# Kernel tuning notes

Hardware: AMD Instinct MI355X
Metric: run time of the kernel (lower is better)

The kernel has to match this reference:

```python
import math
import jax, jax.numpy as jnp
import numpy as np

MAX_T = 300
B, T, V, D, H = 16, 256, 25, 128, 8


def _layernorm(x, g, b):
    m = x.mean(-1, keepdims=True)
    var = ((x - m) ** 2).mean(-1, keepdims=True)
    return (x - m) / jnp.sqrt(var + 1e-5) * g + b


def setup_inputs() -> dict:
    key = jax.random.key(0)
    ks = jax.random.split(key, 8)
    d = D // H
    init = lambda k, shape: jax.random.normal(k, shape, dtype=jnp.float32) * 0.02
    return dict(
        x=jax.random.normal(ks[0], (B, T, V, D), dtype=jnp.float32),
        ln1_g=jnp.ones((D,), jnp.float32), ln1_b=jnp.zeros((D,), jnp.float32),
        qkv_w=init(ks[1], (D, 3 * D)), qkv_b=jnp.zeros((3 * D,), jnp.float32),
        proj_w=init(ks[2], (D, D)), proj_b=jnp.zeros((D,), jnp.float32),
        logit_scale=jnp.full((H, 1, 1), math.log(math.sqrt(d)), dtype=jnp.float32),
        rel_pos_bias=init(ks[3], (H, 2 * MAX_T - 1)),
        ln2_g=jnp.ones((D,), jnp.float32), ln2_b=jnp.zeros((D,), jnp.float32),
        ffn_w1=init(ks[4], (D, 4 * D)), ffn_b1=jnp.zeros((4 * D,), jnp.float32),
        ffn_w2=init(ks[5], (4 * D, D)), ffn_b2=jnp.zeros((D,), jnp.float32),
    )


def reference(x, ln1_g, ln1_b, qkv_w, qkv_b, proj_w, proj_b, logit_scale,
              rel_pos_bias, ln2_g, ln2_b, ffn_w1, ffn_b1, ffn_w2, ffn_b2):
    b, t, v_, dm = x.shape
    h = logit_scale.shape[0]
    d = dm // h
    # (B, T, V, D) -> (B*V, T, D): attention runs over frames per joint
    xf = x.transpose(0, 2, 1, 3).reshape(b * v_, t, dm)
    res = xf
    xn = _layernorm(xf, ln1_g, ln1_b)
    qkv = (xn @ qkv_w + qkv_b).reshape(b * v_, t, 3, h, d).transpose(2, 0, 3, 1, 4)
    q, k, v = qkv[0], qkv[1], qkv[2]  # (BV, h, T, d)
    scale = jnp.exp(jnp.minimum(logit_scale, math.log(100.0)))  # (h,1,1)
    qn = q / jnp.maximum(jnp.linalg.norm(q, axis=-1, keepdims=True), 1e-12) * scale
    kn = k / jnp.maximum(jnp.linalg.norm(k, axis=-1, keepdims=True), 1e-12)
    # learned relative-position bias, gathered to (h, T, T)
    coords = jnp.arange(t)
    rel = coords[:, None] - coords[None, :] + (MAX_T - 1)
    bias = rel_pos_bias[:, rel]
    # SDPA applies its default 1/sqrt(head_dim) scale on top of logit_scale
    scores = jnp.einsum('bhtd,bhsd->bhts', qn, kn) / math.sqrt(d) + bias[None]
    attn = jax.nn.softmax(scores, axis=-1)
    out = jnp.einsum('bhts,bhsd->bhtd', attn, v)
    out = out.transpose(0, 2, 1, 3).reshape(b * v_, t, dm)
    xf = res + (out @ proj_w + proj_b)
    y = _layernorm(xf, ln2_g, ln2_b)
    y = jax.nn.gelu(y @ ffn_w1 + ffn_b1, approximate=False) @ ffn_w2 + ffn_b2
    xf = xf + y
    return xf.reshape(b, v_, t, dm).transpose(0, 2, 1, 3)
```

## Files before the change

### kernel.cpp

```cpp
#include <hip/hip_runtime.h>
#include <hip/hip_fp16.h>
#include <math.h>

#define B_   16
#define T_   256
#define V_   25
#define D_   128
#define H_   8
#define DH   16
#define BV_  (B_*V_)
#define MAXT 300
#define NREL (2*MAXT-1)
#define LOG2E 1.44269504088896f

typedef __attribute__((ext_vector_type(8))) short short8;
typedef __attribute__((ext_vector_type(4))) float f32x4;
typedef __attribute__((ext_vector_type(2))) __fp16 fp16x2;
typedef __attribute__((ext_vector_type(4))) _Float16 half4;
typedef __attribute__((ext_vector_type(8))) _Float16 half8;

__device__ inline short f2bf(float f) {
  union { float f; unsigned u; } a; a.f = f;
  unsigned r = (a.u + 0x7FFF + ((a.u >> 16) & 1)) >> 16;
  return (short)r;
}

__device__ inline float fast_exp2(float x) {
#if __has_builtin(__builtin_amdgcn_exp2f)
  return __builtin_amdgcn_exp2f(x);
#else
  return exp2f(x);
#endif
}

__device__ inline float gelu_fast(float u) {
  float s = u * fmaf(0.0713548162726f, u*u, 1.5957691216057f);
  return u * __builtin_amdgcn_rcpf(1.0f + __expf(-s));
}

__global__ __launch_bounds__(256) void k0_prep(
    const float* __restrict__ qkv_w, const float* __restrict__ pw,
    const float* __restrict__ w1,    const float* __restrict__ w2,
    short* __restrict__ qkv_wt, short* __restrict__ pwt,
    _Float16* __restrict__ w1t, _Float16* __restrict__ w2t)
{
  int i = blockIdx.x*256 + threadIdx.x;
  if (i < 384*128) { int n = i >> 7, k = i & 127; qkv_wt[i] = f2bf(qkv_w[k*384 + n]); }
  if (i < 128*128) { int n = i >> 7, k = i & 127; pwt[i]    = f2bf(pw[k*128 + n]); }
  if (i < 512*128) { int n = i >> 7, k = i & 127; w1t[i]    = (_Float16)w1[k*512 + n]; }
  if (i < 128*512) {
    int r = i & 3, lane = (i >> 2) & 63, hn = (i >> 8) & 31, ot = i >> 13;
    int k = hn*16 + (lane >> 4)*4 + r;
    int n = ot*16 + (lane & 15);
    w2t[i] = (_Float16)w2[k*128 + n];
  }
}

__global__ __launch_bounds__(256) void k1_ln_qkv(
    const float* __restrict__ x, const float* __restrict__ g1, const float* __restrict__ b1,
    const short* __restrict__ qkv_wt, const float* __restrict__ qkv_b,
    const float* __restrict__ logit_scale,
    _Float16* __restrict__ qb, _Float16* __restrict__ kb, _Float16* __restrict__ vt)
{
  __shared__ short xn[64][136];
  const int tid = threadIdx.x;
  const int bv  = blockIdx.x / (T_/64);
  const int t0  = (blockIdx.x % (T_/64)) * 64;
  const int b   = bv / V_, v = bv % V_;

  {
    const int j = tid & 15;
    float4 gA = *(const float4*)(g1 + j*8), gB = *(const float4*)(g1 + j*8 + 4);
    float4 bA = *(const float4*)(b1 + j*8), bB = *(const float4*)(b1 + j*8 + 4);
    float gg[8] = {gA.x,gA.y,gA.z,gA.w,gB.x,gB.y,gB.z,gB.w};
    float bb[8] = {bA.x,bA.y,bA.z,bA.w,bB.x,bB.y,bB.z,bB.w};
    for (int rep = 0; rep < 4; ++rep) {
      const int tok = rep*16 + (tid >> 4);
      const float* xp = x + (((size_t)b*T_ + (t0+tok))*V_ + v)*D_ + j*8;
      float4 a0 = *(const float4*)xp;
      float4 a1 = *(const float4*)(xp+4);
      float e[8] = {a0.x,a0.y,a0.z,a0.w,a1.x,a1.y,a1.z,a1.w};
      float s = 0.f;
      #pragma unroll
      for (int q = 0; q < 8; ++q) s += e[q];
      #pragma unroll
      for (int m = 1; m < 16; m <<= 1) s += __shfl_xor(s, m, 16);
      float mean = s * (1.0f/128.0f);
      float s2 = 0.f;
      #pragma unroll
      for (int q = 0; q < 8; ++q) { float d = e[q]-mean; s2 += d*d; }
      #pragma unroll
      for (int m = 1; m < 16; m <<= 1) s2 += __shfl_xor(s2, m, 16);
      float rstd = rsqrtf(s2*(1.0f/128.0f) + 1e-5f);
      short8 o;
      #pragma unroll
      for (int q = 0; q < 8; ++q) o[q] = f2bf((e[q]-mean)*rstd*gg[q] + bb[q]);
      *(short8*)&xn[tok][j*8] = o;
    }
  }
  __syncthreads();

  const int wave = tid >> 6, lane = tid & 63;
  const int col = lane & 15, quad = lane >> 4;
  short8 af[4][4];
  #pragma unroll
  for (int tt = 0; tt < 4; ++tt)
    #pragma unroll
    for (int kk = 0; kk < 4; ++kk)
      af[tt][kk] = *(const short8*)&xn[tt*16+col][kk*32 + quad*8];

  for (int it = 0; it < 6; ++it) {
    const int tile = wave*6 + it;
    const int n0 = tile*16;
    short8 bf[4];
    #pragma unroll
    for (int kk = 0; kk < 4; ++kk)
      bf[kk] = *(const short8*)(qkv_wt + (size_t)(n0+col)*128 + kk*32 + quad*8);
    f32x4 acc[4] = {{0.f,0.f,0.f,0.f},{0.f,0.f,0.f,0.f},{0.f,0.f,0.f,0.f},{0.f,0.f,0.f,0.f}};
    #pragma unroll
    for (int kk = 0; kk < 4; ++kk)
      #pragma unroll
      for (int tt = 0; tt < 4; ++tt)
        acc[tt] = __builtin_amdgcn_mfma_f32_16x16x32_bf16(af[tt][kk], bf[kk], acc[tt], 0, 0, 0);
    const float bias = qkv_b[n0+col];
    const int h = tile & 7;
    const size_t bh = (size_t)bv*H_ + h;
    if (tile < 16) {
      const float scale = (tile < 8)
        ? __expf(fminf(logit_scale[h], 4.605170185988091f)) * 0.25f * LOG2E : 1.0f;
      #pragma unroll
      for (int tt = 0; tt < 4; ++tt) {
        float val[4], inv[4];
        #pragma unroll
        for (int r = 0; r < 4; ++r) {
          val[r] = acc[tt][r] + bias;
          float s = val[r]*val[r];
          #pragma unroll
          for (int m = 1; m < 16; m <<= 1) s += __shfl_xor(s, m, 16);
          inv[r] = 1.0f / fmaxf(sqrtf(s), 1e-12f);
        }
        const size_t obase = (bh*T_ + (t0 + tt*16 + quad*4))*DH + col;
        if (tile < 8) {
          #pragma unroll
          for (int r = 0; r < 4; ++r) qb[obase + (size_t)r*DH] = (_Float16)(val[r]*inv[r]*scale);
        } else {
          #pragma unroll
          for (int r = 0; r < 4; ++r) kb[obase + (size_t)r*DH] = (_Float16)(val[r]*inv[r]);
        }
      }
    } else {
      #pragma unroll
      for (int tt = 0; tt < 4; ++tt) {
        half4 vh;
        #pragma unroll
        for (int r = 0; r < 4; ++r) vh[r] = (_Float16)(acc[tt][r] + bias);
        *(half4*)(vt + bh*4096 + (size_t)(t0/16 + tt)*256 + col*16 + quad*4) = vh;
      }
    }
  }
}

__global__ __launch_bounds__(256) void k2_attn(
    const float* __restrict__ rel_pos_bias,
    const _Float16* __restrict__ qb, const _Float16* __restrict__ kb,
    const _Float16* __restrict__ vt, short* __restrict__ xattn)
{
  __shared__ float bias_s[NREL + 1];
  const int tid = threadIdx.x;
  const int bh  = blockIdx.x;
  const int h   = bh & (H_-1);
  const int bv  = bh >> 3;
  for (int j = tid; j < NREL; j += 256) bias_s[j] = rel_pos_bias[h*NREL + j] * LOG2E;
  __syncthreads();

  const int wave = tid >> 6, lane = tid & 63;
  const int nn = lane & 15, quad = lane >> 4;
  const size_t qkbase = (size_t)bh * (T_*DH);
  const size_t vbase  = (size_t)bh * 4096;

  half4 qf[4];
  #pragma unroll
  for (int tt = 0; tt < 4; ++tt)
    qf[tt] = *(const half4*)(qb + qkbase + (size_t)(wave*64 + tt*16 + nn)*DH + quad*4);

  f32x4 o[4];
  #pragma unroll
  for (int tt = 0; tt < 4; ++tt) o[tt] = (f32x4){0.f,0.f,0.f,0.f};
  float lsum[4] = {0.f,0.f,0.f,0.f};

  half4 kf = *(const half4*)(kb + qkbase + (size_t)nn*DH + quad*4);
  half4 vf = *(const half4*)(vt + vbase + (size_t)nn*16 + quad*4);

  for (int s16 = 0; s16 < 16; ++s16) {
    half4 kf_n, vf_n;
    if (s16 < 15) {
      kf_n = *(const half4*)(kb + qkbase + (size_t)((s16+1)*16 + nn)*DH + quad*4);
      vf_n = *(const half4*)(vt + vbase + (size_t)(s16+1)*256 + nn*16 + quad*4);
    }
    #pragma unroll
    for (int tt = 0; tt < 4; ++tt) {
      f32x4 c = {0.f,0.f,0.f,0.f};
      c = __builtin_amdgcn_mfma_f32_16x16x16f16(kf, qf[tt], c, 0, 0, 0);
      const int ib = (wave*64 + tt*16 + nn) - (s16*16 + quad*4) + (MAXT-1);
      float p0 = fast_exp2(c[0] + bias_s[ib]);
      float p1 = fast_exp2(c[1] + bias_s[ib - 1]);
      float p2 = fast_exp2(c[2] + bias_s[ib - 2]);
      float p3 = fast_exp2(c[3] + bias_s[ib - 3]);
      lsum[tt] += (p0 + p1) + (p2 + p3);
      fp16x2 lo = __builtin_amdgcn_cvt_pkrtz(p0, p1);
      fp16x2 hi = __builtin_amdgcn_cvt_pkrtz(p2, p3);
      union { struct { fp16x2 a, b; } p; half4 h; } cv;
      cv.p.a = lo; cv.p.b = hi;
      o[tt] = __builtin_amdgcn_mfma_f32_16x16x16f16(cv.h, vf, o[tt], 0, 0, 0);
    }
    kf = kf_n; vf = vf_n;
  }

  #pragma unroll
  for (int tt = 0; tt < 4; ++tt) {
    float l = lsum[tt];
    l += __shfl_xor(l, 16);
    l += __shfl_xor(l, 32);
    float rinv = 1.0f / l;
    #pragma unroll
    for (int r = 0; r < 4; ++r) {
      float inv = __shfl(rinv, quad*4 + r, 16);
      const int t = wave*64 + tt*16 + quad*4 + r;
      xattn[((size_t)bv*T_ + t)*D_ + h*DH + nn] = f2bf(o[tt][r] * inv);
    }
  }
}

__global__ __launch_bounds__(256) void k3_proj(
    const float* __restrict__ x, const short* __restrict__ xattn,
    const short* __restrict__ pwt, const float* __restrict__ proj_b,
    float* __restrict__ xf2)
{
  const int tid = threadIdx.x;
  const int bv  = blockIdx.x / (T_/64);
  const int t0  = (blockIdx.x % (T_/64)) * 64;
  const int b   = bv / V_, v = bv % V_;
  const int wave = tid >> 6, lane = tid & 63;
  const int col = lane & 15, quad = lane >> 4;

  short8 af[4][4];
  #pragma unroll
  for (int tt = 0; tt < 4; ++tt)
    #pragma unroll
    for (int kk = 0; kk < 4; ++kk)
      af[tt][kk] = *(const short8*)(xattn
                    + ((size_t)bv*T_ + t0 + tt*16 + col)*D_ + kk*32 + quad*8);

  for (int it = 0; it < 2; ++it) {
    const int n0 = (wave*2 + it)*16;
    short8 bf[4];
    #pragma unroll
    for (int kk = 0; kk < 4; ++kk)
      bf[kk] = *(const short8*)(pwt + (size_t)(n0+col)*128 + kk*32 + quad*8);
    f32x4 acc[4] = {{0.f,0.f,0.f,0.f},{0.f,0.f,0.f,0.f},{0.f,0.f,0.f,0.f},{0.f,0.f,0.f,0.f}};
    #pragma unroll
    for (int kk = 0; kk < 4; ++kk)
      #pragma unroll
      for (int tt = 0; tt < 4; ++tt)
        acc[tt] = __builtin_amdgcn_mfma_f32_16x16x32_bf16(af[tt][kk], bf[kk], acc[tt], 0, 0, 0);
    const float pbv = proj_b[n0+col];
    #pragma unroll
    for (int tt = 0; tt < 4; ++tt)
      #pragma unroll
      for (int r = 0; r < 4; ++r) {
        const int t = t0 + tt*16 + quad*4 + r;
        float res = x[(((size_t)b*T_ + t)*V_ + v)*D_ + n0 + col];
        xf2[((size_t)bv*T_ + t)*D_ + n0 + col] = acc[tt][r] + pbv + res;
      }
  }
}

__global__ __launch_bounds__(256) void k4_ffn(
    const float* __restrict__ xf2, const float* __restrict__ g2, const float* __restrict__ b2,
    const _Float16* __restrict__ w1t, const float* __restrict__ fb1,
    const _Float16* __restrict__ w2t, const float* __restrict__ fb2,
    float* __restrict__ out)
{
  __shared__ __align__(16) char smem[34816];
  _Float16 (*y_s)[136] = (_Float16 (*)[136])smem;
  _Float16 (*w1c)[136] = (_Float16 (*)[136])smem;
  _Float16 *w2c = (_Float16*)(smem + 64*136*2);

  const int tid = threadIdx.x;
  const int bv  = blockIdx.x / (T_/128);
  const int t0  = (blockIdx.x % (T_/128)) * 128;
  const int b   = bv / V_, v = bv % V_;

  half8 p_w1[4], p_w2[4];
  #pragma unroll
  for (int j = 0; j < 4; ++j) {
    const int u = j*256 + tid;
    p_w1[j] = *(const half8*)(w1t + (size_t)(u >> 4)*128 + (u & 15)*8);
    p_w2[j] = *(const half8*)(w2t + (size_t)((u >> 7)*32 + ((u >> 5) & 3))*256 + (u & 31)*8);
  }

  {
    const int j = tid & 15;
    float4 gA = *(const float4*)(g2 + j*8), gB = *(const float4*)(g2 + j*8 + 4);
    float4 bA = *(const float4*)(b2 + j*8), bB = *(const float4*)(b2 + j*8 + 4);
    float gg[8] = {gA.x,gA.y,gA.z,gA.w,gB.x,gB.y,gB.z,gB.w};
    float bb[8] = {bA.x,bA.y,bA.z,bA.w,bB.x,bB.y,bB.z,bB.w};
    for (int rep = 0; rep < 8; ++rep) {
      const int tok = rep*16 + (tid >> 4);
      const float* xp = xf2 + ((size_t)bv*T_ + t0+tok)*D_ + j*8;
      float4 a0 = *(const float4*)xp;
      float4 a1 = *(const float4*)(xp+4);
      float e[8] = {a0.x,a0.y,a0.z,a0.w,a1.x,a1.y,a1.z,a1.w};
      float s = 0.f;
      #pragma unroll
      for (int q = 0; q < 8; ++q) s += e[q];
      #pragma unroll
      for (int m = 1; m < 16; m <<= 1) s += __shfl_xor(s, m, 16);
      float mean = s * (1.0f/128.0f);
      float s2 = 0.f;
      #pragma unroll
      for (int q = 0; q < 8; ++q) { float d = e[q]-mean; s2 += d*d; }
      #pragma unroll
      for (int m = 1; m < 16; m <<= 1) s2 += __shfl_xor(s2, m, 16);
      float rstd = rsqrtf(s2*(1.0f/128.0f) + 1e-5f);
      half8 o;
      #pragma unroll
      for (int q = 0; q < 8; ++q) o[q] = (_Float16)((e[q]-mean)*rstd*gg[q] + bb[q]);
      *(half8*)&y_s[tok][j*8] = o;
    }
  }
  __syncthreads();

  const int wave = tid >> 6, lane = tid & 63;
  const int col = lane & 15, quad = lane >> 4;

  half8 yf[2][4];
  #pragma unroll
  for (int tt = 0; tt < 2; ++tt)
    #pragma unroll
    for (int kk = 0; kk < 4; ++kk)
      yf[tt][kk] = *(const half8*)&y_s[wave*32 + tt*16 + col][kk*32 + quad*8];
  __syncthreads();

  f32x4 acc2[2][8];
  #pragma unroll
  for (int tt = 0; tt < 2; ++tt)
    #pragma unroll
    for (int ot = 0; ot < 8; ++ot) acc2[tt][ot] = (f32x4){0.f,0.f,0.f,0.f};

  for (int c = 0; c < 8; ++c) {
    #pragma unroll
    for (int j = 0; j < 4; ++j) {
      const int u = j*256 + tid;
      *(half8*)&w1c[u >> 4][(u & 15)*8] = p_w1[j];
      *(half8*)&w2c[(size_t)u*8]        = p_w2[j];
    }
    __syncthreads();

    if (c < 7) {
      #pragma unroll
      for (int j = 0; j < 4; ++j) {
        const int u = j*256 + tid;
        p_w1[j] = *(const half8*)(w1t + (size_t)((c+1)*64 + (u >> 4))*128 + (u & 15)*8);
        p_w2[j] = *(const half8*)(w2t + (size_t)((u >> 7)*32 + (c+1)*4 + ((u >> 5) & 3))*256 + (u & 31)*8);
      }
    }

    #pragma unroll
    for (int ht = 0; ht < 4; ++ht) {
      half8 w1f[4];
      #pragma unroll
      for (int kk = 0; kk < 4; ++kk)
        w1f[kk] = *(const half8*)&w1c[ht*16+col][kk*32 + quad*8];
      f32x4 c0 = {0.f,0.f,0.f,0.f}, c1 = {0.f,0.f,0.f,0.f};
      #pragma unroll
      for (int kk = 0; kk < 4; ++kk) {
        c0 = __builtin_amdgcn_mfma_f32_16x16x32_f16(w1f[kk], yf[0][kk], c0, 0, 0, 0);
        c1 = __builtin_amdgcn_mfma_f32_16x16x32_f16(w1f[kk], yf[1][kk], c1, 0, 0, 0);
      }
      const int hn = c*4 + ht;
      const f32x4 b1v = *(const f32x4*)(fb1 + hn*16 + quad*4);
      half4 pa0, pa1;
      #pragma unroll
      for (int r = 0; r < 4; ++r) {
        pa0[r] = (_Float16)gelu_fast(c0[r] + b1v[r]);
        pa1[r] = (_Float16)gelu_fast(c1[r] + b1v[r]);
      }
      #pragma unroll
      for (int ot = 0; ot < 8; ++ot) {
        half4 w2f = *(const half4*)&w2c[((ot*4 + ht)*64 + lane)*4];
        acc2[0][ot] = __builtin_amdgcn_mfma_f32_16x16x16f16(pa0, w2f, acc2[0][ot], 0, 0, 0);
        acc2[1][ot] = __builtin_amdgcn_mfma_f32_16x16x16f16(pa1, w2f, acc2[1][ot], 0, 0, 0);
      }
    }
    __syncthreads();
  }

  const int tw = t0 + wave*32;
  #pragma unroll
  for (int tt = 0; tt < 2; ++tt)
    #pragma unroll
    for (int ot = 0; ot < 8; ++ot) {
      const float bo = fb2[ot*16 + col];
      #pragma unroll
      for (int r = 0; r < 4; ++r) {
        const int t = tw + tt*16 + quad*4 + r;
        float val = acc2[tt][ot][r] + bo + xf2[((size_t)bv*T_ + t)*D_ + ot*16 + col];
        out[(((size_t)b*T_ + t)*V_ + v)*D_ + ot*16 + col] = val;
      }
    }
}

extern "C" void kernel_launch(void* const* d_in, const int* in_sizes, int n_in,
                              void* d_out, int out_size, void* d_ws, size_t ws_size,
                              hipStream_t stream)
{
  (void)in_sizes; (void)n_in; (void)out_size; (void)ws_size;
  const float* x     = (const float*)d_in[0];
  const float* g1    = (const float*)d_in[1];
  const float* b1    = (const float*)d_in[2];
  const float* qkv_w = (const float*)d_in[3];
  const float* qkv_b = (const float*)d_in[4];
  const float* pw    = (const float*)d_in[5];
  const float* pb    = (const float*)d_in[6];
  const float* ls    = (const float*)d_in[7];
  const float* rpb   = (const float*)d_in[8];
  const float* g2    = (const float*)d_in[9];
  const float* b2    = (const float*)d_in[10];
  const float* w1    = (const float*)d_in[11];
  const float* fb1   = (const float*)d_in[12];
  const float* w2    = (const float*)d_in[13];
  const float* fb2   = (const float*)d_in[14];
  float* out = (float*)d_out;

  const size_t n = (size_t)BV_*T_*D_;
  char* ws = (char*)d_ws;
  _Float16* qb  = (_Float16*)ws;
  _Float16* kb  = (_Float16*)(ws + n*2);
  float*    xf2 = (float*)(ws + n*4);
  _Float16* vt  = (_Float16*)(ws + n*8);
  short*    xab = (short*)(ws + n*10);
  short*    qkv_wt = (short*)(ws + n*12);
  short*    pwt    = qkv_wt + 384*128;
  _Float16* w1t    = (_Float16*)(pwt + 128*128);
  _Float16* w2t    = w1t + 512*128;

  k0_prep  <<<256,          dim3(256), 0, stream>>>(qkv_w, pw, w1, w2, qkv_wt, pwt, w1t, w2t);
  k1_ln_qkv<<<BV_*(T_/64),  dim3(256), 0, stream>>>(x, g1, b1, qkv_wt, qkv_b, ls, qb, kb, vt);
  k2_attn  <<<BV_*H_,       dim3(256), 0, stream>>>(rpb, qb, kb, vt, xab);
  k3_proj  <<<BV_*(T_/64),  dim3(256), 0, stream>>>(x, xab, pwt, pb, xf2);
  k4_ffn   <<<BV_*(T_/128), dim3(256), 0, stream>>>(xf2, g2, b2, w1t, fb1, w2t, fb2, out);
}
```

Measured before the change: 315.1 us.

## Stream FFN weights directly from global into registers instead of staging in LDS

The FFN kernel no longer stages W1/W2 chunks through shared memory with block-wide barriers. Each wave now loads its weight fragments straight from global (L2-resident) memory into registers, double-buffered one hidden tile ahead, which removes LDS writes and reads and the per-chunk __syncthreads. The trade-off is that every wave fetches the same weights separately, so global/L2 traffic and register pressure go up. Separately, the QKV kernel interleaves output tiles across waves (it*4+wave) instead of giving each wave a contiguous range.

```diff
diff --git a/kernel.cpp b/kernel.cpp
--- a/kernel.cpp
+++ b/kernel.cpp
@@ -110,7 +110,7 @@
       af[tt][kk] = *(const short8*)&xn[tt*16+col][kk*32 + quad*8];
 
   for (int it = 0; it < 6; ++it) {
-    const int tile = wave*6 + it;
+    const int tile = it*4 + wave;
     const int n0 = tile*16;
     short8 bf[4];
     #pragma unroll
@@ -281,23 +281,11 @@
     const _Float16* __restrict__ w2t, const float* __restrict__ fb2,
     float* __restrict__ out)
 {
-  __shared__ __align__(16) char smem[34816];
-  _Float16 (*y_s)[136] = (_Float16 (*)[136])smem;
-  _Float16 (*w1c)[136] = (_Float16 (*)[136])smem;
-  _Float16 *w2c = (_Float16*)(smem + 64*136*2);
-
+  __shared__ _Float16 y_s[128][136];
   const int tid = threadIdx.x;
   const int bv  = blockIdx.x / (T_/128);
   const int t0  = (blockIdx.x % (T_/128)) * 128;
   const int b   = bv / V_, v = bv % V_;
-
-  half8 p_w1[4], p_w2[4];
-  #pragma unroll
-  for (int j = 0; j < 4; ++j) {
-    const int u = j*256 + tid;
-    p_w1[j] = *(const half8*)(w1t + (size_t)(u >> 4)*128 + (u & 15)*8);
-    p_w2[j] = *(const half8*)(w2t + (size_t)((u >> 7)*32 + ((u >> 5) & 3))*256 + (u & 31)*8);
-  }
 
   {
     const int j = tid & 15;
@@ -340,7 +328,6 @@
     #pragma unroll
     for (int kk = 0; kk < 4; ++kk)
       yf[tt][kk] = *(const half8*)&y_s[wave*32 + tt*16 + col][kk*32 + quad*8];
-  __syncthreads();
 
   f32x4 acc2[2][8];
   #pragma unroll
@@ -348,52 +335,44 @@
     #pragma unroll
     for (int ot = 0; ot < 8; ++ot) acc2[tt][ot] = (f32x4){0.f,0.f,0.f,0.f};
 
-  for (int c = 0; c < 8; ++c) {
-    #pragma unroll
-    for (int j = 0; j < 4; ++j) {
-      const int u = j*256 + tid;
-      *(half8*)&w1c[u >> 4][(u & 15)*8] = p_w1[j];
-      *(half8*)&w2c[(size_t)u*8]        = p_w2[j];
-    }
-    __syncthreads();
-
-    if (c < 7) {
-      #pragma unroll
-      for (int j = 0; j < 4; ++j) {
-        const int u = j*256 + tid;
-        p_w1[j] = *(const half8*)(w1t + (size_t)((c+1)*64 + (u >> 4))*128 + (u & 15)*8);
-        p_w2[j] = *(const half8*)(w2t + (size_t)((u >> 7)*32 + (c+1)*4 + ((u >> 5) & 3))*256 + (u & 31)*8);
-      }
-    }
-
-    #pragma unroll
-    for (int ht = 0; ht < 4; ++ht) {
-      half8 w1f[4];
-      #pragma unroll
-      for (int kk = 0; kk < 4; ++kk)
-        w1f[kk] = *(const half8*)&w1c[ht*16+col][kk*32 + quad*8];
-      f32x4 c0 = {0.f,0.f,0.f,0.f}, c1 = {0.f,0.f,0.f,0.f};
-      #pragma unroll
-      for (int kk = 0; kk < 4; ++kk) {
-        c0 = __builtin_amdgcn_mfma_f32_16x16x32_f16(w1f[kk], yf[0][kk], c0, 0, 0, 0);
-        c1 = __builtin_amdgcn_mfma_f32_16x16x32_f16(w1f[kk], yf[1][kk], c1, 0, 0, 0);
-      }
-      const int hn = c*4 + ht;
-      const f32x4 b1v = *(const f32x4*)(fb1 + hn*16 + quad*4);
-      half4 pa0, pa1;
-      #pragma unroll
-      for (int r = 0; r < 4; ++r) {
-        pa0[r] = (_Float16)gelu_fast(c0[r] + b1v[r]);
-        pa1[r] = (_Float16)gelu_fast(c1[r] + b1v[r]);
-      }
-      #pragma unroll
-      for (int ot = 0; ot < 8; ++ot) {
-        half4 w2f = *(const half4*)&w2c[((ot*4 + ht)*64 + lane)*4];
-        acc2[0][ot] = __builtin_amdgcn_mfma_f32_16x16x16f16(pa0, w2f, acc2[0][ot], 0, 0, 0);
-        acc2[1][ot] = __builtin_amdgcn_mfma_f32_16x16x16f16(pa1, w2f, acc2[1][ot], 0, 0, 0);
-      }
-    }
-    __syncthreads();
+  half8 w1a[4], w1b[4];
+  half4 w2a[8], w2b[8];
+
+  auto LOADW = [&](int hn, half8 (&w1d)[4], half4 (&w2d)[8]) {
+    #pragma unroll
+    for (int kk = 0; kk < 4; ++kk)
+      w1d[kk] = *(const half8*)(w1t + (size_t)(hn*16+col)*128 + kk*32 + quad*8);
+    #pragma unroll
+    for (int ot = 0; ot < 8; ++ot)
+      w2d[ot] = *(const half4*)(w2t + ((size_t)(ot*32 + hn)*64 + lane)*4);
+  };
+  auto BODY = [&](int hn, half8 (&w1f)[4], half4 (&w2f)[8],
+                  half8 (&w1n)[4], half4 (&w2n)[8]) {
+    if (hn + 1 < 32) LOADW(hn + 1, w1n, w2n);
+    f32x4 c0 = {0.f,0.f,0.f,0.f}, c1 = {0.f,0.f,0.f,0.f};
+    #pragma unroll
+    for (int kk = 0; kk < 4; ++kk) {
+      c0 = __builtin_amdgcn_mfma_f32_16x16x32_f16(w1f[kk], yf[0][kk], c0, 0, 0, 0);
+      c1 = __builtin_amdgcn_mfma_f32_16x16x32_f16(w1f[kk], yf[1][kk], c1, 0, 0, 0);
+    }
+    const f32x4 b1v = *(const f32x4*)(fb1 + hn*16 + quad*4);
+    half4 pa0, pa1;
+    #pragma unroll
+    for (int r = 0; r < 4; ++r) {
+      pa0[r] = (_Float16)gelu_fast(c0[r] + b1v[r]);
+      pa1[r] = (_Float16)gelu_fast(c1[r] + b1v[r]);
+    }
+    #pragma unroll
+    for (int ot = 0; ot < 8; ++ot) {
+      acc2[0][ot] = __builtin_amdgcn_mfma_f32_16x16x16f16(pa0, w2f[ot], acc2[0][ot], 0, 0, 0);
+      acc2[1][ot] = __builtin_amdgcn_mfma_f32_16x16x16f16(pa1, w2f[ot], acc2[1][ot], 0, 0, 0);
+    }
+  };
+
+  LOADW(0, w1a, w2a);
+  for (int hn = 0; hn < 32; hn += 2) {
+    BODY(hn,     w1a, w2a, w1b, w2b);
+    BODY(hn + 1, w1b, w2b, w1a, w2a);
   }
 
   const int tw = t0 + wave*32;
```

Result: slower. 363.9 us (+15.5%).
